# Performance work log

Measured on AMD Instinct MI355X. Metric: run time of the kernel, lower is better.

The kernel has to match this reference:

```python
import jax, jax.numpy as jnp
import numpy as np

N = 1024          # n_particles
D = 3             # n_spatial_dims
HID = 256         # hidden_size
H = 4             # heads
HD = HID // H     # per-head dim = pairwise feature dim (64)
DEPTH = 4
DIM = N * D       # 3072 (input/output dim)
MLP_IN = DIM + HD + 1
EPS = 1e-5        # eqx.nn.RMSNorm default eps

# static unique-pair indices (repeat=False -> upper triangle, i<j)
I_IDX, J_IDX = np.triu_indices(N, k=1)


def _linear_init(k, out_f, in_f):
    kw, kb = jax.random.split(k)
    lim = 1.0 / np.sqrt(in_f)
    W = jax.random.uniform(kw, (out_f, in_f), minval=-lim, maxval=lim, dtype=jnp.float32)
    b = jax.random.uniform(kb, (out_f,), minval=-lim, maxval=lim, dtype=jnp.float32)
    return W, b


def setup_inputs() -> dict:
    key = jax.random.key(0)
    ks = jax.random.split(key, 12)
    Wk, bk = _linear_init(ks[0], HD * H, 1)   # key_proj
    Wv, bv = _linear_init(ks[1], HD, 1)       # value_proj
    Wq, bq = _linear_init(ks[2], HD * H, 1)   # time_dist_proj
    W0, b0 = _linear_init(ks[3], HID, MLP_IN)
    Wh = jnp.stack([_linear_init(ks[4 + i], HID, HID)[0] for i in range(DEPTH - 1)])
    bh = jnp.stack([_linear_init(ks[4 + i], HID, HID)[1] for i in range(DEPTH - 1)])
    Wout, bout = _linear_init(ks[7], DIM, HID)
    g = jnp.ones((DEPTH, HID), dtype=jnp.float32)  # RMSNorm weights
    x = jax.random.normal(ks[8], (DIM,), dtype=jnp.float32)
    t = jax.random.uniform(ks[9], (1,), dtype=jnp.float32)
    return {"x": x, "t": t, "Wk": Wk, "bk": bk, "Wv": Wv, "bv": bv,
            "Wq": Wq, "bq": bq, "W0": W0, "b0": b0, "Wh": Wh, "bh": bh,
            "Wout": Wout, "bout": bout, "g": g}


def _rmsnorm(h, gw):
    return h * jax.lax.rsqrt(jnp.mean(h * h) + EPS) * gw


def reference(x, t, Wk, bk, Wv, bv, Wq, bq, W0, b0, Wh, bh, Wout, bout, g):
    # --- compute_distances: unique pairwise distances, P = N(N-1)/2 ---
    x3 = x.reshape(N, D)
    diff = x3[I_IDX] - x3[J_IDX]                       # (P, D)
    dists = jnp.sqrt(jnp.sum(diff * diff, axis=-1))    # (P,)

    # --- EfficientPairwiseInteraction (Linear with 1 input = scale + bias) ---
    keys = dists[:, None] * Wk[:, 0][None, :] + bk     # (P, H*HD)
    values = dists[:, None] * Wv[:, 0][None, :] + bv   # (P, HD)
    q = Wq[:, 0] * t[0] + bq                           # (H*HD,)

    kh = keys.reshape(-1, H, HD)                       # contiguous split per head
    qh = q.reshape(H, HD)
    logits = jnp.einsum('phd,hd->hp', kh, qh)          # (H, P)
    attn = jax.nn.softmax(logits, axis=-1)             # softmax over pairs per head
    pair_feat = jnp.einsum('hp,pd->d', attn, values)   # sum over heads of attn_h @ values

    # --- MLP with RMSNorm (rms_norm=True), gelu activation ---
    feats = jnp.concatenate([x, pair_feat, t])         # (MLP_IN,)
    h = jax.nn.gelu(_rmsnorm(feats @ W0.T + b0, g[0]))
    for i in range(DEPTH - 1):
        h = jax.nn.gelu(_rmsnorm(h @ Wh[i].T + bh[i], g[i + 1]))
    return h @ Wout.T + bout                           # (DIM,)
```

## Files before the change

### kernel.cpp

```cpp
#include <hip/hip_runtime.h>
#include <math.h>

#define NB 256
#define TPB 256
#define NMLP 16
#define MERGER 255
#define EPS 1e-5f
#define LOG2E 1.4426950408889634f

typedef unsigned long long u64;

#define SL_PART 0
#define SL_Z0   4096
#define SL_Z1   8192
#define SL_Z2   12288
#define SL_Z3   16384
#define SLOT_LINES 5120

__device__ __forceinline__ float gelu_fast(float v) {
    float u = 0.7978845608028654f * (v + 0.044715f * v * v * v);
    float e = __expf(2.0f * u);
    return 0.5f * v * (2.0f - 2.0f / (e + 1.0f));
}

__device__ __forceinline__ void pin(float v) { asm volatile("" :: "v"(v)); }

__device__ __forceinline__ void push_slot(u64* p, float x) {
    u64 v = (1ull << 32) | (u64)__float_as_uint(x);
    __hip_atomic_store(p, v, __ATOMIC_RELAXED, __HIP_MEMORY_SCOPE_AGENT);
}
__device__ __forceinline__ float poll_slot(const u64* p) {
    u64 v = __hip_atomic_load(p, __ATOMIC_RELAXED, __HIP_MEMORY_SCOPE_AGENT);
    int n = 0;
    while ((v >> 32) != 1ull) {
        if (++n < 4) __builtin_amdgcn_s_sleep(1);
        else __builtin_amdgcn_s_sleep(16);
        v = __hip_atomic_load(p, __ATOMIC_RELAXED, __HIP_MEMORY_SCOPE_AGENT);
    }
    return __uint_as_float((unsigned)(v & 0xffffffffull));
}

__device__ __forceinline__ float block_sum_all(float v, float* sc, int lane, int wave) {
    for (int o = 32; o; o >>= 1) v += __shfl_xor(v, o);
    __syncthreads();
    if (lane == 0) sc[wave] = v;
    __syncthreads();
    return sc[0] + sc[1] + sc[2] + sc[3];
}

__global__ __launch_bounds__(TPB, 1) void vf_fused(
    const float* __restrict__ x, const float* __restrict__ t,
    const float* __restrict__ Wk, const float* __restrict__ Wv,
    const float* __restrict__ bv, const float* __restrict__ Wq,
    const float* __restrict__ bq,
    const float* __restrict__ W0, const float* __restrict__ b0,
    const float* __restrict__ Wh, const float* __restrict__ bh,
    const float* __restrict__ Wout, const float* __restrict__ bout,
    const float* __restrict__ g, float* __restrict__ out, float* __restrict__ wsf) {

    __shared__ float xs[3072];
    __shared__ float hs[TPB];
    __shared__ float sc[32];
    u64* slots = (u64*)wsf;
    const int tid = threadIdx.x;
    const int bid = blockIdx.x;
    const int lane = tid & 63, wave = tid >> 6;

    if (tid < 20) {
        int line = bid * 20 + tid;
        if (line < SLOT_LINES) {
            u64 v = __hip_atomic_load(slots + (u64)line * 16,
                                      __ATOMIC_RELAXED, __HIP_MEMORY_SCOPE_AGENT);
            asm volatile("" :: "v"((unsigned)v));
        }
    }

    float gg0 = g[tid], gg1 = g[256 + tid], gg2 = g[512 + tid], gg3 = g[768 + tid];
    float b0v = b0[bid];
    float t0 = t[0];
    float wvv = (tid < 64) ? Wv[tid] : 0.f;
    float bvv = (tid < 64) ? bv[tid] : 0.f;
    float w0r[13];
    #pragma unroll
    for (int k = 0; k < 12; ++k) w0r[k] = W0[bid * 3137 + tid + k * 256];
    w0r[12] = (tid < 65) ? W0[bid * 3137 + 3072 + tid] : 0.f;
    float wor[12], bor[3];
    #pragma unroll
    for (int k = 0; k < 3; ++k) {
        int r = bid * 12 + wave * 3 + k;
        bor[k] = bout[r];
        #pragma unroll
        for (int q = 0; q < 4; ++q) wor[k * 4 + q] = Wout[r * 256 + lane + 64 * q];
    }
    const int mr = tid >> 4, mcg = tid & 15;
    const int mR = bid * 16 + mr;
    float wmr[48], bhv0 = 0.f, bhv1 = 0.f, bhv2 = 0.f;
    if (bid < NMLP) {
        #pragma unroll
        for (int l = 0; l < 3; ++l)
            #pragma unroll
            for (int k = 0; k < 16; ++k)
                wmr[l * 16 + k] = Wh[l * 65536 + mR * 256 + mcg * 16 + k];
        bhv0 = bh[mR]; bhv1 = bh[256 + mR]; bhv2 = bh[512 + mR];
    }

    for (int i = tid; i < 3072; i += TPB) xs[i] = x[i];

    float qv = Wq[tid] * t0 + bq[tid];
    float prod = Wk[tid] * qv;
    for (int o = 32; o; o >>= 1) prod += __shfl_xor(prod, o);
    __syncthreads();
    if (lane == 0) sc[wave] = prod;
    __syncthreads();
    float c2[4];
    #pragma unroll
    for (int h = 0; h < 4; ++h) c2[h] = sc[h] * LOG2E;
    __syncthreads();

    const int i0 = bid * 4 + wave;
    float xi0 = xs[3 * i0], xi1 = xs[3 * i0 + 1], xi2 = xs[3 * i0 + 2];
    float dreg[16];
    float tmax = -INFINITY, tmin = INFINITY;
    #pragma unroll
    for (int e = 0; e < 16; ++e) {
        int j = lane + 64 * e;
        float dx = xi0 - xs[3 * j], dy = xi1 - xs[3 * j + 1], dz = xi2 - xs[3 * j + 2];
        float d = sqrtf(dx * dx + dy * dy + dz * dz);
        dreg[e] = d;
        if (j != i0) { tmax = fmaxf(tmax, d); tmin = fminf(tmin, d); }
    }
    for (int o = 32; o; o >>= 1) {
        tmax = fmaxf(tmax, __shfl_xor(tmax, o));
        tmin = fminf(tmin, __shfl_xor(tmin, o));
    }
    if (lane == 0) { sc[wave] = tmax; sc[8 + wave] = tmin; }
    __syncthreads();
    float bmax = fmaxf(fmaxf(sc[0], sc[1]), fmaxf(sc[2], sc[3]));
    float bmin = fminf(fminf(sc[8], sc[9]), fminf(sc[10], sc[11]));
    float m2[4];
    #pragma unroll
    for (int h = 0; h < 4; ++h) m2[h] = (c2[h] >= 0.f) ? c2[h] * bmax : c2[h] * bmin;

    float se[4] = {0, 0, 0, 0}, sd[4] = {0, 0, 0, 0};
    #pragma unroll
    for (int e = 0; e < 16; ++e) {
        int j = lane + 64 * e;
        if (j == i0) continue;
        float d = dreg[e];
        #pragma unroll
        for (int h = 0; h < 4; ++h) {
            float ee = exp2f(c2[h] * d - m2[h]);
            se[h] += ee;
            sd[h] += d * ee;
        }
    }
    for (int o = 32; o; o >>= 1) {
        #pragma unroll
        for (int h = 0; h < 4; ++h) { se[h] += __shfl_xor(se[h], o); sd[h] += __shfl_xor(sd[h], o); }
    }
    __syncthreads();
    if (lane == 0) {
        #pragma unroll
        for (int h = 0; h < 4; ++h) { sc[wave * 8 + h] = se[h]; sc[wave * 8 + 4 + h] = sd[h]; }
    }
    __syncthreads();
    if (tid < 4) push_slot(slots + SL_PART + bid * 16 + tid, m2[tid]);
    else if (tid < 8) {
        int h = tid - 4;
        push_slot(slots + SL_PART + bid * 16 + tid, sc[h] + sc[8 + h] + sc[16 + h] + sc[24 + h]);
    } else if (tid < 12) {
        int h = tid - 8;
        push_slot(slots + SL_PART + bid * 16 + tid, sc[4 + h] + sc[12 + h] + sc[20 + h] + sc[28 + h]);
    }

    float acc = 0.f;
    #pragma unroll
    for (int k = 0; k < 12; ++k) acc += w0r[k] * xs[tid + k * 256];
    float Pc = (tid < 64) ? w0r[12] * wvv : 0.f;
    float Qc = (tid < 64) ? 4.0f * w0r[12] * bvv : ((tid == 64) ? w0r[12] * t0 : 0.f);
    for (int o = 32; o; o >>= 1) {
        acc += __shfl_xor(acc, o);
        Pc += __shfl_xor(Pc, o);
        Qc += __shfl_xor(Qc, o);
    }
    __syncthreads();
    if (lane == 0) { sc[wave] = acc; sc[8 + wave] = Pc; sc[16 + wave] = Qc; }
    __syncthreads();
    float Pb = sc[8] + sc[9] + sc[10] + sc[11];
    float zS = (sc[0] + sc[1] + sc[2] + sc[3]) + (sc[16] + sc[17] + sc[18] + sc[19]) + b0v;
    if (tid == 0) {
        push_slot(slots + SL_PART + bid * 16 + 12, Pb);
        push_slot(slots + SL_PART + bid * 16 + 13, zS);
    }

    if (bid == MERGER) {
        float pv[12];
        {
            u64 vv[12];
            const u64* base = slots + SL_PART + (u64)tid * 16;
            bool ready;
            do {
                ready = true;
                #pragma unroll
                for (int k = 0; k < 12; ++k) {
                    vv[k] = __hip_atomic_load(base + k, __ATOMIC_RELAXED, __HIP_MEMORY_SCOPE_AGENT);
                    ready &= (vv[k] >> 32) == 1ull;
                }
                if (!ready) __builtin_amdgcn_s_sleep(1);
            } while (!ready);
            #pragma unroll
            for (int k = 0; k < 12; ++k) pv[k] = __uint_as_float((unsigned)(vv[k] & 0xffffffffull));
        }
        float pm[4] = {pv[0], pv[1], pv[2], pv[3]};
        float pse[4] = {pv[4], pv[5], pv[6], pv[7]};
        float psd[4] = {pv[8], pv[9], pv[10], pv[11]};
        float pmr[4] = {pm[0], pm[1], pm[2], pm[3]};
        for (int o = 32; o; o >>= 1) {
            #pragma unroll
            for (int h = 0; h < 4; ++h) pmr[h] = fmaxf(pmr[h], __shfl_xor(pmr[h], o));
        }
        __syncthreads();
        if (lane == 0) {
            #pragma unroll
            for (int h = 0; h < 4; ++h) sc[wave * 4 + h] = pmr[h];
        }
        __syncthreads();
        float gm[4];
        #pragma unroll
        for (int h = 0; h < 4; ++h)
            gm[h] = fmaxf(fmaxf(sc[h], sc[4 + h]), fmaxf(sc[8 + h], sc[12 + h]));
        float s8[8];
        #pragma unroll
        for (int h = 0; h < 4; ++h) {
            float scl = exp2f(pm[h] - gm[h]);
            s8[h] = pse[h] * scl;
            s8[4 + h] = psd[h] * scl;
        }
        for (int o = 32; o; o >>= 1) {
            #pragma unroll
            for (int k = 0; k < 8; ++k) s8[k] += __shfl_xor(s8[k], o);
        }
        __syncthreads();
        if (lane == 0) {
            #pragma unroll
            for (int k = 0; k < 8; ++k) sc[wave * 8 + k] = s8[k];
        }
        __syncthreads();
        float s_tot = 0.f;
        #pragma unroll
        for (int h = 0; h < 4; ++h) {
            float seh = sc[h] + sc[8 + h] + sc[16 + h] + sc[24 + h];
            float sdh = sc[4 + h] + sc[12 + h] + sc[20 + h] + sc[28 + h];
            s_tot += sdh / seh;
        }
        float Pbr = poll_slot(slots + SL_PART + (u64)tid * 16 + 12);
        float zSr = poll_slot(slots + SL_PART + (u64)tid * 16 + 13);
        push_slot(slots + SL_Z0 + tid * 16, fmaf(s_tot, Pbr, zSr));
    }

    if (bid < NMLP) {
        #pragma unroll
        for (int k = 0; k < 48; ++k) pin(wmr[k]);
        pin(bhv0); pin(bhv1); pin(bhv2); pin(gg0); pin(gg1); pin(gg2);

        {
            float zv = poll_slot(slots + SL_Z0 + tid * 16);
            float ssum = block_sum_all(zv * zv, sc, lane, wave);
            float hv = gelu_fast(zv * rsqrtf(ssum * (1.f / 256.f) + EPS) * gg0);
            hs[tid] = hv;
            __syncthreads();
            float a = 0.f;
            #pragma unroll
            for (int k = 0; k < 16; ++k) a += wmr[k] * hs[mcg * 16 + k];
            for (int o = 8; o; o >>= 1) a += __shfl_xor(a, o);
            if (mcg == 0) push_slot(slots + SL_Z1 + mR * 16, a + bhv0);
        }
        {
            float zv = poll_slot(slots + SL_Z1 + tid * 16);
            float ssum = block_sum_all(zv * zv, sc, lane, wave);
            float hv = gelu_fast(zv * rsqrtf(ssum * (1.f / 256.f) + EPS) * gg1);
            hs[tid] = hv;
            __syncthreads();
            float a = 0.f;
            #pragma unroll
            for (int k = 0; k < 16; ++k) a += wmr[16 + k] * hs[mcg * 16 + k];
            for (int o = 8; o; o >>= 1) a += __shfl_xor(a, o);
            if (mcg == 0) push_slot(slots + SL_Z2 + mR * 16, a + bhv1);
        }
        {
            float zv = poll_slot(slots + SL_Z2 + tid * 16);
            float ssum = block_sum_all(zv * zv, sc, lane, wave);
            float hv = gelu_fast(zv * rsqrtf(ssum * (1.f / 256.f) + EPS) * gg2);
            hs[tid] = hv;
            __syncthreads();
            float a = 0.f;
            #pragma unroll
            for (int k = 0; k < 16; ++k) a += wmr[32 + k] * hs[mcg * 16 + k];
            for (int o = 8; o; o >>= 1) a += __shfl_xor(a, o);
            if (mcg == 0) {
                float val = a + bhv2;
                #pragma unroll
                for (int c = 0; c < 16; ++c)
                    push_slot(slots + SL_Z3 + c * 4096 + mR * 16, val);
            }
        }
    }

    #pragma unroll
    for (int k = 0; k < 12; ++k) pin(wor[k]);
    pin(bor[0]); pin(bor[1]); pin(bor[2]); pin(gg3);

    {
        float zv = poll_slot(slots + SL_Z3 + (bid & 15) * 4096 + tid * 16);
        float ssum = block_sum_all(zv * zv, sc, lane, wave);
        float hv = gelu_fast(zv * rsqrtf(ssum * (1.f / 256.f) + EPS) * gg3);
        hs[tid] = hv;
        __syncthreads();
        #pragma unroll
        for (int k = 0; k < 3; ++k) {
            float a = 0.f;
            #pragma unroll
            for (int q = 0; q < 4; ++q) a += wor[k * 4 + q] * hs[lane + 64 * q];
            for (int o = 32; o; o >>= 1) a += __shfl_xor(a, o);
            if (lane == 0) out[bid * 12 + wave * 3 + k] = a + bor[k];
        }
    }
}

extern "C" void kernel_launch(void* const* d_in, const int* in_sizes, int n_in,
                              void* d_out, int out_size, void* d_ws, size_t ws_size,
                              hipStream_t stream) {
    const float* x = (const float*)d_in[0];
    const float* t = (const float*)d_in[1];
    const float* Wk = (const float*)d_in[2];
    const float* Wv = (const float*)d_in[4];
    const float* bv = (const float*)d_in[5];
    const float* Wq = (const float*)d_in[6];
    const float* bq = (const float*)d_in[7];
    const float* W0 = (const float*)d_in[8];
    const float* b0 = (const float*)d_in[9];
    const float* Wh = (const float*)d_in[10];
    const float* bh = (const float*)d_in[11];
    const float* Wout = (const float*)d_in[12];
    const float* bout = (const float*)d_in[13];
    const float* g = (const float*)d_in[14];
    float* out = (float*)d_out;
    float* wsf = (float*)d_ws;

    vf_fused<<<NB, TPB, 0, stream>>>(x, t, Wk, Wv, bv, Wq, bq, W0, b0, Wh, bh,
                                     Wout, bout, g, out, wsf);
}
```

Measured before the change: 19.73 us.

## Concentrate pairwise attention and first-layer work into 64 producer blocks

Blocks that compute pairwise-distance softmax partials and first-layer dot products drop from 256 to 64. Each producer now handles 16 particle rows (4 per wave) and 4 W0 rows instead of 1. The merger moves to block 64 and does a single-wave reduction over 64 partials, which removes several block-level syncs. Preload of the slot lines and per-block W0 register caching are removed. The aim is to cut cross-block flag traffic and merger latency, at the cost of more serial work per producer block and more register pressure from dreg[4][16].

```diff
diff --git a/kernel.cpp b/kernel.cpp
--- a/kernel.cpp
+++ b/kernel.cpp
@@ -3,19 +3,20 @@
 
 #define NB 256
 #define TPB 256
+#define NPROD 64
 #define NMLP 16
-#define MERGER 255
+#define MERGER 64
 #define EPS 1e-5f
 #define LOG2E 1.4426950408889634f
 
 typedef unsigned long long u64;
 
 #define SL_PART 0
-#define SL_Z0   4096
-#define SL_Z1   8192
-#define SL_Z2   12288
-#define SL_Z3   16384
-#define SLOT_LINES 5120
+#define SL_ZP   1024
+#define SL_Z0   5120
+#define SL_Z1   9216
+#define SL_Z2   13312
+#define SL_Z3   17408
 
 __device__ __forceinline__ float gelu_fast(float v) {
     float u = 0.7978845608028654f * (v + 0.044715f * v * v * v);
@@ -61,29 +62,13 @@
     __shared__ float xs[3072];
     __shared__ float hs[TPB];
     __shared__ float sc[32];
+    __shared__ float sbc;
     u64* slots = (u64*)wsf;
     const int tid = threadIdx.x;
     const int bid = blockIdx.x;
     const int lane = tid & 63, wave = tid >> 6;
 
-    if (tid < 20) {
-        int line = bid * 20 + tid;
-        if (line < SLOT_LINES) {
-            u64 v = __hip_atomic_load(slots + (u64)line * 16,
-                                      __ATOMIC_RELAXED, __HIP_MEMORY_SCOPE_AGENT);
-            asm volatile("" :: "v"((unsigned)v));
-        }
-    }
-
-    float gg0 = g[tid], gg1 = g[256 + tid], gg2 = g[512 + tid], gg3 = g[768 + tid];
-    float b0v = b0[bid];
-    float t0 = t[0];
-    float wvv = (tid < 64) ? Wv[tid] : 0.f;
-    float bvv = (tid < 64) ? bv[tid] : 0.f;
-    float w0r[13];
-    #pragma unroll
-    for (int k = 0; k < 12; ++k) w0r[k] = W0[bid * 3137 + tid + k * 256];
-    w0r[12] = (tid < 65) ? W0[bid * 3137 + 3072 + tid] : 0.f;
+    float gg3 = g[768 + tid];
     float wor[12], bor[3];
     #pragma unroll
     for (int k = 0; k < 3; ++k) {
@@ -95,6 +80,7 @@
     const int mr = tid >> 4, mcg = tid & 15;
     const int mR = bid * 16 + mr;
     float wmr[48], bhv0 = 0.f, bhv1 = 0.f, bhv2 = 0.f;
+    float gg0 = 0.f, gg1 = 0.f, gg2 = 0.f;
     if (bid < NMLP) {
         #pragma unroll
         for (int l = 0; l < 3; ++l)
@@ -102,160 +88,181 @@
             for (int k = 0; k < 16; ++k)
                 wmr[l * 16 + k] = Wh[l * 65536 + mR * 256 + mcg * 16 + k];
         bhv0 = bh[mR]; bhv1 = bh[256 + mR]; bhv2 = bh[512 + mR];
-    }
-
-    for (int i = tid; i < 3072; i += TPB) xs[i] = x[i];
-
-    float qv = Wq[tid] * t0 + bq[tid];
-    float prod = Wk[tid] * qv;
-    for (int o = 32; o; o >>= 1) prod += __shfl_xor(prod, o);
-    __syncthreads();
-    if (lane == 0) sc[wave] = prod;
-    __syncthreads();
-    float c2[4];
-    #pragma unroll
-    for (int h = 0; h < 4; ++h) c2[h] = sc[h] * LOG2E;
-    __syncthreads();
-
-    const int i0 = bid * 4 + wave;
-    float xi0 = xs[3 * i0], xi1 = xs[3 * i0 + 1], xi2 = xs[3 * i0 + 2];
-    float dreg[16];
-    float tmax = -INFINITY, tmin = INFINITY;
-    #pragma unroll
-    for (int e = 0; e < 16; ++e) {
-        int j = lane + 64 * e;
-        float dx = xi0 - xs[3 * j], dy = xi1 - xs[3 * j + 1], dz = xi2 - xs[3 * j + 2];
-        float d = sqrtf(dx * dx + dy * dy + dz * dz);
-        dreg[e] = d;
-        if (j != i0) { tmax = fmaxf(tmax, d); tmin = fminf(tmin, d); }
-    }
-    for (int o = 32; o; o >>= 1) {
-        tmax = fmaxf(tmax, __shfl_xor(tmax, o));
-        tmin = fminf(tmin, __shfl_xor(tmin, o));
-    }
-    if (lane == 0) { sc[wave] = tmax; sc[8 + wave] = tmin; }
-    __syncthreads();
-    float bmax = fmaxf(fmaxf(sc[0], sc[1]), fmaxf(sc[2], sc[3]));
-    float bmin = fminf(fminf(sc[8], sc[9]), fminf(sc[10], sc[11]));
-    float m2[4];
-    #pragma unroll
-    for (int h = 0; h < 4; ++h) m2[h] = (c2[h] >= 0.f) ? c2[h] * bmax : c2[h] * bmin;
-
-    float se[4] = {0, 0, 0, 0}, sd[4] = {0, 0, 0, 0};
-    #pragma unroll
-    for (int e = 0; e < 16; ++e) {
-        int j = lane + 64 * e;
-        if (j == i0) continue;
-        float d = dreg[e];
-        #pragma unroll
-        for (int h = 0; h < 4; ++h) {
-            float ee = exp2f(c2[h] * d - m2[h]);
-            se[h] += ee;
-            sd[h] += d * ee;
-        }
-    }
-    for (int o = 32; o; o >>= 1) {
-        #pragma unroll
-        for (int h = 0; h < 4; ++h) { se[h] += __shfl_xor(se[h], o); sd[h] += __shfl_xor(sd[h], o); }
-    }
-    __syncthreads();
-    if (lane == 0) {
-        #pragma unroll
-        for (int h = 0; h < 4; ++h) { sc[wave * 8 + h] = se[h]; sc[wave * 8 + 4 + h] = sd[h]; }
-    }
-    __syncthreads();
-    if (tid < 4) push_slot(slots + SL_PART + bid * 16 + tid, m2[tid]);
-    else if (tid < 8) {
-        int h = tid - 4;
-        push_slot(slots + SL_PART + bid * 16 + tid, sc[h] + sc[8 + h] + sc[16 + h] + sc[24 + h]);
-    } else if (tid < 12) {
-        int h = tid - 8;
-        push_slot(slots + SL_PART + bid * 16 + tid, sc[4 + h] + sc[12 + h] + sc[20 + h] + sc[28 + h]);
-    }
-
-    float acc = 0.f;
-    #pragma unroll
-    for (int k = 0; k < 12; ++k) acc += w0r[k] * xs[tid + k * 256];
-    float Pc = (tid < 64) ? w0r[12] * wvv : 0.f;
-    float Qc = (tid < 64) ? 4.0f * w0r[12] * bvv : ((tid == 64) ? w0r[12] * t0 : 0.f);
-    for (int o = 32; o; o >>= 1) {
-        acc += __shfl_xor(acc, o);
-        Pc += __shfl_xor(Pc, o);
-        Qc += __shfl_xor(Qc, o);
-    }
-    __syncthreads();
-    if (lane == 0) { sc[wave] = acc; sc[8 + wave] = Pc; sc[16 + wave] = Qc; }
-    __syncthreads();
-    float Pb = sc[8] + sc[9] + sc[10] + sc[11];
-    float zS = (sc[0] + sc[1] + sc[2] + sc[3]) + (sc[16] + sc[17] + sc[18] + sc[19]) + b0v;
-    if (tid == 0) {
-        push_slot(slots + SL_PART + bid * 16 + 12, Pb);
-        push_slot(slots + SL_PART + bid * 16 + 13, zS);
+        gg0 = g[tid]; gg1 = g[256 + tid]; gg2 = g[512 + tid];
+    }
+
+    if (bid < NPROD) {
+        float t0 = t[0];
+        float wvv = (tid < 64) ? Wv[tid] : 0.f;
+        float bvv = (tid < 64) ? bv[tid] : 0.f;
+
+        for (int i = tid; i < 3072; i += TPB) xs[i] = x[i];
+
+        float qv = Wq[tid] * t0 + bq[tid];
+        float prod = Wk[tid] * qv;
+        for (int o = 32; o; o >>= 1) prod += __shfl_xor(prod, o);
+        __syncthreads();
+        if (lane == 0) sc[wave] = prod;
+        __syncthreads();
+        float c2[4];
+        #pragma unroll
+        for (int h = 0; h < 4; ++h) c2[h] = sc[h] * LOG2E;
+        __syncthreads();
+
+        const int rowbase = bid * 16 + wave * 4;
+        float dreg[4][16];
+        float tmax = -INFINITY, tmin = INFINITY;
+        #pragma unroll
+        for (int rr = 0; rr < 4; ++rr) {
+            int i0 = rowbase + rr;
+            float xi0 = xs[3 * i0], xi1 = xs[3 * i0 + 1], xi2 = xs[3 * i0 + 2];
+            #pragma unroll
+            for (int e = 0; e < 16; ++e) {
+                int j = lane + 64 * e;
+                float dx = xi0 - xs[3 * j], dy = xi1 - xs[3 * j + 1], dz = xi2 - xs[3 * j + 2];
+                float d = sqrtf(dx * dx + dy * dy + dz * dz);
+                dreg[rr][e] = d;
+                if (j != i0) { tmax = fmaxf(tmax, d); tmin = fminf(tmin, d); }
+            }
+        }
+        for (int o = 32; o; o >>= 1) {
+            tmax = fmaxf(tmax, __shfl_xor(tmax, o));
+            tmin = fminf(tmin, __shfl_xor(tmin, o));
+        }
+        if (lane == 0) { sc[wave] = tmax; sc[8 + wave] = tmin; }
+        __syncthreads();
+        float bmax = fmaxf(fmaxf(sc[0], sc[1]), fmaxf(sc[2], sc[3]));
+        float bmin = fminf(fminf(sc[8], sc[9]), fminf(sc[10], sc[11]));
+        float m2[4];
+        #pragma unroll
+        for (int h = 0; h < 4; ++h) m2[h] = (c2[h] >= 0.f) ? c2[h] * bmax : c2[h] * bmin;
+
+        float se[4] = {0, 0, 0, 0}, sd[4] = {0, 0, 0, 0};
+        #pragma unroll
+        for (int rr = 0; rr < 4; ++rr) {
+            int i0 = rowbase + rr;
+            #pragma unroll
+            for (int e = 0; e < 16; ++e) {
+                int j = lane + 64 * e;
+                if (j == i0) continue;
+                float d = dreg[rr][e];
+                #pragma unroll
+                for (int h = 0; h < 4; ++h) {
+                    float ee = exp2f(c2[h] * d - m2[h]);
+                    se[h] += ee;
+                    sd[h] += d * ee;
+                }
+            }
+        }
+        for (int o = 32; o; o >>= 1) {
+            #pragma unroll
+            for (int h = 0; h < 4; ++h) { se[h] += __shfl_xor(se[h], o); sd[h] += __shfl_xor(sd[h], o); }
+        }
+        __syncthreads();
+        if (lane == 0) {
+            #pragma unroll
+            for (int h = 0; h < 4; ++h) { sc[wave * 8 + h] = se[h]; sc[wave * 8 + 4 + h] = sd[h]; }
+        }
+        __syncthreads();
+        if (tid < 4) push_slot(slots + SL_PART + bid * 16 + tid, m2[tid]);
+        else if (tid < 8) {
+            int h = tid - 4;
+            push_slot(slots + SL_PART + bid * 16 + tid, sc[h] + sc[8 + h] + sc[16 + h] + sc[24 + h]);
+        } else if (tid < 12) {
+            int h = tid - 8;
+            push_slot(slots + SL_PART + bid * 16 + tid, sc[4 + h] + sc[12 + h] + sc[20 + h] + sc[28 + h]);
+        }
+
+        float a4[4], p4[4], q4[4];
+        #pragma unroll
+        for (int rr = 0; rr < 4; ++rr) {
+            const float* row = W0 + (u64)(bid * 4 + rr) * 3137;
+            float a = 0.f;
+            #pragma unroll
+            for (int k = 0; k < 12; ++k) a += row[tid + k * 256] * xs[tid + k * 256];
+            float w12 = (tid < 65) ? row[3072 + tid] : 0.f;
+            a4[rr] = a;
+            p4[rr] = (tid < 64) ? w12 * wvv : 0.f;
+            q4[rr] = (tid < 64) ? 4.0f * w12 * bvv : ((tid == 64) ? w12 * t0 : 0.f);
+        }
+        #pragma unroll
+        for (int rr = 0; rr < 4; ++rr) {
+            float a = a4[rr], p = p4[rr], q = q4[rr];
+            for (int o = 32; o; o >>= 1) {
+                a += __shfl_xor(a, o);
+                p += __shfl_xor(p, o);
+                q += __shfl_xor(q, o);
+            }
+            __syncthreads();
+            if (lane == 0) { sc[wave] = a; sc[8 + wave] = p; sc[16 + wave] = q; }
+            __syncthreads();
+            if (tid == 0) {
+                int r = bid * 4 + rr;
+                float Pb = sc[8] + sc[9] + sc[10] + sc[11];
+                float zS = (sc[0] + sc[1] + sc[2] + sc[3]) +
+                           (sc[16] + sc[17] + sc[18] + sc[19]) + b0[r];
+                push_slot(slots + SL_ZP + r * 16 + 0, zS);
+                push_slot(slots + SL_ZP + r * 16 + 1, Pb);
+            }
+        }
     }
 
     if (bid == MERGER) {
-        float pv[12];
+        float s_tot = 0.f;
+        if (tid < 64) {
+            float pv[12];
+            {
+                u64 vv[12];
+                const u64* base = slots + SL_PART + (u64)tid * 16;
+                bool ready;
+                do {
+                    ready = true;
+                    #pragma unroll
+                    for (int k = 0; k < 12; ++k) {
+                        vv[k] = __hip_atomic_load(base + k, __ATOMIC_RELAXED, __HIP_MEMORY_SCOPE_AGENT);
+                        ready &= (vv[k] >> 32) == 1ull;
+                    }
+                    if (!ready) __builtin_amdgcn_s_sleep(1);
+                } while (!ready);
+                #pragma unroll
+                for (int k = 0; k < 12; ++k) pv[k] = __uint_as_float((unsigned)(vv[k] & 0xffffffffull));
+            }
+            float gm[4] = {pv[0], pv[1], pv[2], pv[3]};
+            for (int o = 32; o; o >>= 1) {
+                #pragma unroll
+                for (int h = 0; h < 4; ++h) gm[h] = fmaxf(gm[h], __shfl_xor(gm[h], o));
+            }
+            float s8[8];
+            #pragma unroll
+            for (int h = 0; h < 4; ++h) {
+                float scl = exp2f(pv[h] - gm[h]);
+                s8[h] = pv[4 + h] * scl;
+                s8[4 + h] = pv[8 + h] * scl;
+            }
+            for (int o = 32; o; o >>= 1) {
+                #pragma unroll
+                for (int k = 0; k < 8; ++k) s8[k] += __shfl_xor(s8[k], o);
+            }
+            #pragma unroll
+            for (int h = 0; h < 4; ++h) s_tot += s8[4 + h] / s8[h];
+        }
+        if (tid == 0) sbc = s_tot;
+        __syncthreads();
+        s_tot = sbc;
         {
-            u64 vv[12];
-            const u64* base = slots + SL_PART + (u64)tid * 16;
+            const u64* base = slots + SL_ZP + (u64)tid * 16;
+            u64 a, b;
             bool ready;
             do {
-                ready = true;
-                #pragma unroll
-                for (int k = 0; k < 12; ++k) {
-                    vv[k] = __hip_atomic_load(base + k, __ATOMIC_RELAXED, __HIP_MEMORY_SCOPE_AGENT);
-                    ready &= (vv[k] >> 32) == 1ull;
-                }
+                a = __hip_atomic_load(base + 0, __ATOMIC_RELAXED, __HIP_MEMORY_SCOPE_AGENT);
+                b = __hip_atomic_load(base + 1, __ATOMIC_RELAXED, __HIP_MEMORY_SCOPE_AGENT);
+                ready = ((a >> 32) == 1ull) && ((b >> 32) == 1ull);
                 if (!ready) __builtin_amdgcn_s_sleep(1);
             } while (!ready);
-            #pragma unroll
-            for (int k = 0; k < 12; ++k) pv[k] = __uint_as_float((unsigned)(vv[k] & 0xffffffffull));
-        }
-        float pm[4] = {pv[0], pv[1], pv[2], pv[3]};
-        float pse[4] = {pv[4], pv[5], pv[6], pv[7]};
-        float psd[4] = {pv[8], pv[9], pv[10], pv[11]};
-        float pmr[4] = {pm[0], pm[1], pm[2], pm[3]};
-        for (int o = 32; o; o >>= 1) {
-            #pragma unroll
-            for (int h = 0; h < 4; ++h) pmr[h] = fmaxf(pmr[h], __shfl_xor(pmr[h], o));
-        }
-        __syncthreads();
-        if (lane == 0) {
-            #pragma unroll
-            for (int h = 0; h < 4; ++h) sc[wave * 4 + h] = pmr[h];
-        }
-        __syncthreads();
-        float gm[4];
-        #pragma unroll
-        for (int h = 0; h < 4; ++h)
-            gm[h] = fmaxf(fmaxf(sc[h], sc[4 + h]), fmaxf(sc[8 + h], sc[12 + h]));
-        float s8[8];
-        #pragma unroll
-        for (int h = 0; h < 4; ++h) {
-            float scl = exp2f(pm[h] - gm[h]);
-            s8[h] = pse[h] * scl;
-            s8[4 + h] = psd[h] * scl;
-        }
-        for (int o = 32; o; o >>= 1) {
-            #pragma unroll
-            for (int k = 0; k < 8; ++k) s8[k] += __shfl_xor(s8[k], o);
-        }
-        __syncthreads();
-        if (lane == 0) {
-            #pragma unroll
-            for (int k = 0; k < 8; ++k) sc[wave * 8 + k] = s8[k];
-        }
-        __syncthreads();
-        float s_tot = 0.f;
-        #pragma unroll
-        for (int h = 0; h < 4; ++h) {
-            float seh = sc[h] + sc[8 + h] + sc[16 + h] + sc[24 + h];
-            float sdh = sc[4 + h] + sc[12 + h] + sc[20 + h] + sc[28 + h];
-            s_tot += sdh / seh;
-        }
-        float Pbr = poll_slot(slots + SL_PART + (u64)tid * 16 + 12);
-        float zSr = poll_slot(slots + SL_PART + (u64)tid * 16 + 13);
-        push_slot(slots + SL_Z0 + tid * 16, fmaf(s_tot, Pbr, zSr));
+            float zS = __uint_as_float((unsigned)(a & 0xffffffffull));
+            float Pb = __uint_as_float((unsigned)(b & 0xffffffffull));
+            push_slot(slots + SL_Z0 + tid * 16, fmaf(s_tot, Pb, zS));
+        }
     }
 
     if (bid < NMLP) {
```

Measured after the change: 28.70 us. 45.5% more time.
